# Performance work log

Hardware: AMD Instinct MI355X
Metric: run time of the kernel (lower is better)

The kernel has to match this reference:

```python
import jax, jax.numpy as jnp
import numpy as np

B, N, D = 4, 2048, 1024

def setup_inputs() -> dict:
    key = jax.random.key(0)
    ks = jax.random.split(key, 8)
    s = 1.0 / np.sqrt(D)
    return {
        "x": jax.random.normal(ks[0], (B, N, D), dtype=jnp.float32),
        "Wq": jax.random.normal(ks[1], (D, D), dtype=jnp.float32) * s,
        "bq": jnp.zeros((D,), dtype=jnp.float32),
        "Wk": jax.random.normal(ks[2], (D, D), dtype=jnp.float32) * s,
        "bk": jnp.zeros((D,), dtype=jnp.float32),
        "Wv": jax.random.normal(ks[3], (D, D), dtype=jnp.float32) * s,
        "bv": jnp.zeros((D,), dtype=jnp.float32),
        "gamma": jnp.ones((1,), dtype=jnp.float32),
    }

def reference(x, Wq, bq, Wk, bk, Wv, bv, gamma):
    d = x.shape[-1]
    delta = 1.0 / jnp.sqrt(jnp.asarray(d, dtype=x.dtype))
    # torch Linear: y = x @ W.T + b, W is [out, in]
    Q = jnp.einsum('bnd,ed->bne', x, Wq) + bq
    K = jnp.einsum('bnd,ed->bne', x, Wk) + bk
    V = jnp.einsum('bnd,ed->bne', x, Wv) + bv
    scores = jnp.einsum('bne,bme->bnm', Q, K) * delta  # [B, N, N]
    attn = jax.nn.softmax(scores, axis=-1)
    out = jnp.einsum('bnm,bme->bne', attn, V)
    return out * gamma + x
```

## Files before the change

### kernel.cpp

```cpp
#include <hip/hip_runtime.h>

typedef _Float16 f16;
typedef __attribute__((ext_vector_type(4))) _Float16 f16x4;
typedef __attribute__((ext_vector_type(8))) _Float16 f16x8;
typedef __attribute__((ext_vector_type(4))) float f32x4;

#define B_ 4
#define N_ 2048
#define D_ 1024

#define FENCE asm volatile("" ::: "memory")

__global__ __launch_bounds__(256) void k_cast_all(const float4* __restrict__ x,
                                                  const float4* __restrict__ wq,
                                                  const float4* __restrict__ wk,
                                                  const float4* __restrict__ wv,
                                                  f16x4* __restrict__ xo,
                                                  f16x4* __restrict__ wqo,
                                                  f16x4* __restrict__ wko,
                                                  f16x4* __restrict__ wvo,
                                                  float* __restrict__ rowsum) {
  int b = blockIdx.x;
  if (b >= 11264) {
    rowsum[(b - 11264) * 256 + threadIdx.x] = 0.f;
    return;
  }
  const float4* in;
  f16x4* out;
  int idx;
  if (b < 8192)       { in = x;  out = xo;  idx = b * 256 + threadIdx.x; }
  else if (b < 9216)  { in = wq; out = wqo; idx = (b - 8192) * 256 + threadIdx.x; }
  else if (b < 10240) { in = wk; out = wko; idx = (b - 9216) * 256 + threadIdx.x; }
  else                { in = wv; out = wvo; idx = (b - 10240) * 256 + threadIdx.x; }
  float4 v = in[idx];
  f16x4 o = { (_Float16)v.x, (_Float16)v.y, (_Float16)v.z, (_Float16)v.w };
  out[idx] = o;
}

__device__ __forceinline__ void stage_half(const char* g0, int ldB, int kByte,
                                           char* slot, int tid) {
#pragma unroll
  for (int r = 0; r < 2; ++r) {
    int lin = r * 8192 + tid * 16;
    int row = lin >> 7;
    int lch = ((lin >> 4) & 7) ^ (row & 7);
    const char* g = g0 + (long)row * ldB + kByte + lch * 16;
    char* l = slot + r * 8192 + ((tid >> 6) << 10);
    __builtin_amdgcn_global_load_lds(
        (const __attribute__((address_space(1))) unsigned int*)g,
        (__attribute__((address_space(3))) unsigned int*)l, 16, 0, 0);
  }
}

__device__ __forceinline__ void gemm256(const char* gA, int ldaB,
                                        const char* gB, int ldbB,
                                        int nK, char* lds, f32x4 acc[2][4][2][2]) {
  const int tid = threadIdx.x;
  const int lane = tid & 63;
  const int wave = tid >> 6;
  const int wm = wave >> 2, wn = wave & 3;
  const int quad = lane >> 4, l16 = lane & 15;
  const int l7 = l16 & 7;
  const char* gA1 = gA + (long)128 * ldaB;
  const char* gB1 = gB + (long)128 * ldbB;
  char* Abuf = lds;
  char* Bbuf = lds + 65536;
  stage_half(gA,  ldaB, 0, Abuf, tid);
  stage_half(gB,  ldbB, 0, Bbuf, tid);
  stage_half(gA1, ldaB, 0, Abuf + 16384, tid);
  stage_half(gB1, ldbB, 0, Bbuf + 16384, tid);
  for (int t = 0; t < nK; ++t) {
    const int c = t & 1;
    char* Ac = Abuf + c * 32768;
    char* Bc = Bbuf + c * 32768;
    char* An = Abuf + (c ^ 1) * 32768;
    char* Bn = Bbuf + (c ^ 1) * 32768;
    const bool st = (t + 1 < nK);
    const int kB = (t + 1) << 7;
    f16x8 bf[2][2];
#pragma unroll
    for (int ph = 0; ph < 4; ++ph) {
      const int Ah = ph & 1, Bh = ph >> 1;
      if (ph == 0)      { asm volatile("s_waitcnt vmcnt(4)" ::: "memory"); }
      else if (ph == 1) { if (st) asm volatile("s_waitcnt vmcnt(4)" ::: "memory");
                          else    asm volatile("s_waitcnt vmcnt(2)" ::: "memory"); }
      else if (ph == 2) { if (st) asm volatile("s_waitcnt vmcnt(4)" ::: "memory");
                          else    asm volatile("s_waitcnt vmcnt(0)" ::: "memory"); }
      __builtin_amdgcn_s_barrier();
      FENCE;
      f16x8 af[4][2];
      const char* Ab = Ac + Ah * 16384;
#pragma unroll
      for (int i = 0; i < 4; ++i) {
        int rA = wm * 64 + i * 16 + l16;
#pragma unroll
        for (int kk = 0; kk < 2; ++kk)
          af[i][kk] = *(const f16x8*)(Ab + rA * 128 + ((((kk << 2) | quad) ^ l7) << 4));
      }
      if (Ah == 0) {
        const char* Bb = Bc + Bh * 16384;
#pragma unroll
        for (int jn = 0; jn < 2; ++jn) {
          int rB = wn * 32 + jn * 16 + l16;
#pragma unroll
          for (int kk = 0; kk < 2; ++kk)
            bf[jn][kk] = *(const f16x8*)(Bb + rB * 128 + ((((kk << 2) | quad) ^ l7) << 4));
        }
      }
      if (st) {
        if (ph == 0)      stage_half(gA,  ldaB, kB, An, tid);
        else if (ph == 1) stage_half(gB,  ldbB, kB, Bn, tid);
        else if (ph == 2) stage_half(gA1, ldaB, kB, An + 16384, tid);
        else              stage_half(gB1, ldbB, kB, Bn + 16384, tid);
      }
      FENCE;
      __builtin_amdgcn_s_barrier();
      __builtin_amdgcn_s_setprio(1);
#pragma unroll
      for (int i = 0; i < 4; ++i)
#pragma unroll
        for (int jn = 0; jn < 2; ++jn)
#pragma unroll
          for (int kk = 0; kk < 2; ++kk)
            acc[Ah][i][Bh][jn] = __builtin_amdgcn_mfma_f32_16x16x32_f16(
                af[i][kk], bf[jn][kk], acc[Ah][i][Bh][jn], 0, 0, 0);
      __builtin_amdgcn_s_setprio(0);
    }
  }
  asm volatile("s_waitcnt vmcnt(0)" ::: "memory");
  __builtin_amdgcn_s_barrier();
  FENCE;
}

__device__ __forceinline__ void gemm_tb(const char* gA, int ldaB,
                                        const char* gB, int ldbB,
                                        int nK, char* lds, f32x4 acc[4][4]) {
  const int tid = threadIdx.x;
  const int lane = tid & 63;
  const int wave = tid >> 6;
  const int wm = wave >> 1, wn = wave & 1;
  const int quad = lane >> 4, l16 = lane & 15;
  const int l7 = l16 & 7;
  const char* gA1 = gA + (long)128 * ldaB;
  stage_half(gA,  ldaB, 0, lds, tid);
  stage_half(gA1, ldaB, 0, lds + 16384, tid);
  stage_half(gB,  ldbB, 0, lds + 32768, tid);
  stage_half(gA,  ldaB, 128, lds + 49152, tid);
  stage_half(gA1, ldaB, 128, lds + 49152 + 16384, tid);
  stage_half(gB,  ldbB, 128, lds + 49152 + 32768, tid);
  int cs = 0;
  for (int t = 0; t < nK; ++t) {
    char* Ac = lds + cs * 49152;
    char* Bc = Ac + 32768;
    int ns = cs + 2; if (ns >= 3) ns -= 3;
    char* An = lds + ns * 49152;
    const bool st = (t + 2 < nK);
    const int kB = (t + 2) << 7;
#pragma unroll
    for (int ph = 0; ph < 2; ++ph) {
      if (ph == 0) {
        if (t + 1 < nK) asm volatile("s_waitcnt vmcnt(6)" ::: "memory");
        else            asm volatile("s_waitcnt vmcnt(0)" ::: "memory");
      }
      __builtin_amdgcn_s_barrier();
      FENCE;
      f16x8 af[4], bf[4];
#pragma unroll
      for (int i = 0; i < 4; ++i) {
        int rA = wm * 64 + i * 16 + l16;
        af[i] = *(const f16x8*)(Ac + rA * 128 + ((((ph << 2) | quad) ^ l7) << 4));
      }
#pragma unroll
      for (int j = 0; j < 4; ++j) {
        int rB = wn * 64 + j * 16 + l16;
        bf[j] = *(const f16x8*)(Bc + rB * 128 + ((((ph << 2) | quad) ^ l7) << 4));
      }
      if (st) {
        if (ph == 0) { stage_half(gA,  ldaB, kB, An, tid);
                       stage_half(gA1, ldaB, kB, An + 16384, tid); }
        else         { stage_half(gB,  ldbB, kB, An + 32768, tid); }
      }
      FENCE;
      __builtin_amdgcn_s_barrier();
      __builtin_amdgcn_s_setprio(1);
#pragma unroll
      for (int i = 0; i < 4; ++i)
#pragma unroll
        for (int j = 0; j < 4; ++j)
          acc[i][j] = __builtin_amdgcn_mfma_f32_16x16x32_f16(af[i], bf[j], acc[i][j], 0, 0, 0);
      __builtin_amdgcn_s_setprio(0);
    }
    cs = cs + 1; if (cs == 3) cs = 0;
  }
  asm volatile("s_waitcnt vmcnt(0)" ::: "memory");
  __builtin_amdgcn_s_barrier();
  FENCE;
}

__global__ __launch_bounds__(512, 2) void k_qkv(const f16* __restrict__ X,
                                                const f16* __restrict__ Wq,
                                                const f16* __restrict__ Wk,
                                                const f16* __restrict__ Wv,
                                                const float* __restrict__ bq,
                                                const float* __restrict__ bk,
                                                const float* __restrict__ bv,
                                                f16* __restrict__ Q, f16* __restrict__ Ko,
                                                f16* __restrict__ Vt) {
  __shared__ __align__(16) char lds[147456];
  int fid = blockIdx.x;
  int xcd = fid & 7, k = fid >> 3;
  int rowt = xcd * 4 + (k & 3);
  int colt = k >> 2;
  int tm = rowt * 256;
  int w = colt >> 3;
  int tnl = (colt & 7) * 128;
  const f16* Wsel = (w == 0) ? Wq : (w == 1) ? Wk : Wv;
  f32x4 acc[4][4];
#pragma unroll
  for (int i = 0; i < 4; ++i)
#pragma unroll
    for (int j = 0; j < 4; ++j) acc[i][j] = (f32x4){0.f, 0.f, 0.f, 0.f};
  gemm_tb((const char*)(X + (long)tm * D_), D_ * 2,
          (const char*)(Wsel + (long)tnl * D_), D_ * 2, D_ / 64, lds, acc);
  const int tid = threadIdx.x;
  const int lane = tid & 63, wave = tid >> 6;
  const int wm = wave >> 1, wn = wave & 1;
  const int quad = lane >> 4, l16 = lane & 15;
  if (w < 2) {
    const float* bias = w ? bk : bq;
    f16* outp = w ? Ko : Q;
#pragma unroll
    for (int j = 0; j < 4; ++j) {
      int col = tnl + wn * 64 + j * 16 + l16;
      float bb = bias[col];
#pragma unroll
      for (int i = 0; i < 4; ++i) {
        int rbase = tm + wm * 64 + i * 16 + quad * 4;
#pragma unroll
        for (int r = 0; r < 4; ++r)
          outp[(long)(rbase + r) * D_ + col] = (_Float16)(acc[i][j][r] + bb);
      }
    }
  } else {
    int bidx = tm >> 11, ntok = tm & 2047;
    f16* VtB = Vt + (long)bidx * D_ * N_ + ntok;
    f16* ldsT = (f16*)lds;
#pragma unroll
    for (int j = 0; j < 4; ++j) {
      int cl = wn * 64 + j * 16 + l16;
      float bb = bv[tnl + cl];
#pragma unroll
      for (int i = 0; i < 4; ++i) {
        int rl = wm * 64 + i * 16 + quad * 4;
        f16x4 p = { (_Float16)(acc[i][j][0] + bb), (_Float16)(acc[i][j][1] + bb),
                    (_Float16)(acc[i][j][2] + bb), (_Float16)(acc[i][j][3] + bb) };
        *(f16x4*)(ldsT + cl * 264 + rl) = p;
      }
    }
    FENCE;
    __builtin_amdgcn_s_barrier();
    FENCE;
#pragma unroll
    for (int p = 0; p < 8; ++p) {
      int f = p * 16 + (tid >> 5);
      int cc = tid & 31;
      f16x8 v = *(const f16x8*)(ldsT + f * 264 + cc * 8);
      *(f16x8*)(VtB + (long)(tnl + f) * N_ + cc * 8) = v;
    }
  }
}

__global__ __launch_bounds__(512, 2) void k_scores(const f16* __restrict__ Qf,
                                                   const f16* __restrict__ Kf,
                                                   f16* __restrict__ S,
                                                   float* __restrict__ rowsum) {
  __shared__ __align__(16) char lds[131072];
  int fid = blockIdx.x;
  int xcd = fid & 7, k = fid >> 3;
  int lin = xcd * 32 + k;
  int b = lin >> 6;
  int t = lin & 63;
  int rowt = t & 7, colt = t >> 3;
  int tm = rowt * 256, tn = colt * 256;
  f32x4 acc[2][4][2][2];
#pragma unroll
  for (int Ah = 0; Ah < 2; ++Ah)
#pragma unroll
    for (int i = 0; i < 4; ++i)
#pragma unroll
      for (int Bh = 0; Bh < 2; ++Bh)
#pragma unroll
        for (int jn = 0; jn < 2; ++jn) acc[Ah][i][Bh][jn] = (f32x4){0.f, 0.f, 0.f, 0.f};
  gemm256((const char*)(Qf + (long)b * N_ * D_ + (long)tm * D_), D_ * 2,
          (const char*)(Kf + (long)b * N_ * D_ + (long)tn * D_), D_ * 2,
          D_ / 64, lds, acc);
  const int tid = threadIdx.x;
  const int lane = tid & 63, wave = tid >> 6;
  const int wm = wave >> 2, wn = wave & 3;
  const int quad = lane >> 4, l16 = lane & 15;
  f16* Sb = S + (long)b * N_ * N_;
  const float delta = 0.03125f;
  f16* ldsS = (f16*)lds;
  float rsum[2][4][4];
#pragma unroll
  for (int Ah = 0; Ah < 2; ++Ah)
#pragma unroll
    for (int i = 0; i < 4; ++i)
#pragma unroll
      for (int r = 0; r < 4; ++r) rsum[Ah][i][r] = 0.f;
#pragma unroll
  for (int Bh = 0; Bh < 2; ++Bh) {
    FENCE;
    __builtin_amdgcn_s_barrier();
    FENCE;
#pragma unroll
    for (int Ah = 0; Ah < 2; ++Ah)
#pragma unroll
      for (int i = 0; i < 4; ++i) {
        int rloc = Ah * 128 + wm * 64 + i * 16 + quad * 4;
#pragma unroll
        for (int jn = 0; jn < 2; ++jn) {
          int col = wn * 32 + jn * 16 + l16;
#pragma unroll
          for (int r = 0; r < 4; ++r) {
            float e = __expf(acc[Ah][i][Bh][jn][r] * delta);
            rsum[Ah][i][r] += e;
            ldsS[(rloc + r) * 136 + col] = (_Float16)e;
          }
        }
      }
    FENCE;
    __builtin_amdgcn_s_barrier();
    FENCE;
#pragma unroll
    for (int p = 0; p < 8; ++p) {
      int row = p * 32 + (tid >> 4);
      int cc = tid & 15;
      f16x8 v = *(const f16x8*)(ldsS + row * 136 + cc * 8);
      *(f16x8*)(Sb + (long)(tm + row) * N_ + tn + Bh * 128 + cc * 8) = v;
    }
  }
#pragma unroll
  for (int m = 1; m < 16; m <<= 1)
#pragma unroll
    for (int Ah = 0; Ah < 2; ++Ah)
#pragma unroll
      for (int i = 0; i < 4; ++i)
#pragma unroll
        for (int r = 0; r < 4; ++r) rsum[Ah][i][r] += __shfl_xor(rsum[Ah][i][r], m);
  if (l16 == 0) {
    float* rs = rowsum + (long)b * N_ + tm;
#pragma unroll
    for (int Ah = 0; Ah < 2; ++Ah)
#pragma unroll
      for (int i = 0; i < 4; ++i)
#pragma unroll
        for (int r = 0; r < 4; ++r)
          atomicAdd(rs + Ah * 128 + wm * 64 + i * 16 + quad * 4 + r, rsum[Ah][i][r]);
  }
}

__global__ __launch_bounds__(512, 2) void k_out(const f16* __restrict__ P,
                                                const f16* __restrict__ Vt,
                                                const f16* __restrict__ xf,
                                                const float* __restrict__ gamma,
                                                const float* __restrict__ rowsum,
                                                float* __restrict__ out) {
  __shared__ __align__(16) char lds[147456];
  int fid = blockIdx.x;
  int xcd = fid & 7, kq = fid >> 3;
  int lin = xcd * 32 + kq;
  int b = lin >> 6;
  int t = lin & 63;
  int rowt = t >> 3, colt = t & 7;
  int tm = rowt * 256, tn = colt * 128;
  f32x4 acc[4][4];
#pragma unroll
  for (int i = 0; i < 4; ++i)
#pragma unroll
    for (int j = 0; j < 4; ++j) acc[i][j] = (f32x4){0.f, 0.f, 0.f, 0.f};
  gemm_tb((const char*)(P + (long)b * N_ * N_ + (long)tm * N_), N_ * 2,
          (const char*)(Vt + (long)b * D_ * N_ + (long)tn * N_), N_ * 2,
          N_ / 64, lds, acc);
  const int tid = threadIdx.x;
  const int lane = tid & 63, wave = tid >> 6;
  const int wm = wave >> 1, wn = wave & 1;
  const int quad = lane >> 4, l16 = lane & 15;
  float g = gamma[0];
  float inv[4][4];
#pragma unroll
  for (int i = 0; i < 4; ++i)
#pragma unroll
    for (int r = 0; r < 4; ++r)
      inv[i][r] = g / rowsum[(long)b * N_ + tm + wm * 64 + i * 16 + quad * 4 + r];
#pragma unroll
  for (int j = 0; j < 4; ++j) {
    int col = tn + wn * 64 + j * 16 + l16;
#pragma unroll
    for (int i = 0; i < 4; ++i) {
      int rbase = tm + wm * 64 + i * 16 + quad * 4;
#pragma unroll
      for (int r = 0; r < 4; ++r) {
        long idx = (long)b * N_ * D_ + (long)(rbase + r) * D_ + col;
        out[idx] = acc[i][j][r] * inv[i][r] + (float)xf[idx];
      }
    }
  }
}

extern "C" void kernel_launch(void* const* d_in, const int* in_sizes, int n_in,
                              void* d_out, int out_size, void* d_ws, size_t ws_size,
                              hipStream_t stream) {
  const float* x  = (const float*)d_in[0];
  const float* Wq = (const float*)d_in[1];
  const float* bq = (const float*)d_in[2];
  const float* Wk = (const float*)d_in[3];
  const float* bk = (const float*)d_in[4];
  const float* Wv = (const float*)d_in[5];
  const float* bv = (const float*)d_in[6];
  const float* gamma = (const float*)d_in[7];
  float* out = (float*)d_out;
  char* ws = (char*)d_ws;

  f16* Qb  = (f16*)(ws);
  f16* Kb  = (f16*)(ws + (16u << 20));
  f16* Vt  = (f16*)(ws + (32u << 20));
  f16* Xb  = (f16*)(ws + (48u << 20));
  f16* Wqb = (f16*)(ws + (64u << 20));
  f16* Wkb = (f16*)(ws + (66u << 20));
  f16* Wvb = (f16*)(ws + (68u << 20));
  f16* S   = (f16*)(ws + (64u << 20));
  float* rowsum = (float*)(ws + (96u << 20));

  k_cast_all<<<11296, 256, 0, stream>>>((const float4*)x, (const float4*)Wq,
                                        (const float4*)Wk, (const float4*)Wv,
                                        (f16x4*)Xb, (f16x4*)Wqb, (f16x4*)Wkb, (f16x4*)Wvb,
                                        rowsum);
  k_qkv<<<768, 512, 0, stream>>>(Xb, Wqb, Wkb, Wvb, bq, bk, bv, Qb, Kb, Vt);
  k_scores<<<256, 512, 0, stream>>>(Qb, Kb, S, rowsum);
  k_out<<<256, 512, 0, stream>>>(S, Vt, Xb, gamma, rowsum, out);
}
```

Baseline: 250.1 us.

## Use 256x256 tiles for QKV and split-K output GEMM with atomics

Drops the 256x128 triple-buffered gemm_tb and moves k_qkv and k_out onto the 256x256 gemm256 path, halving the QKV grid. k_out now splits K into two halves (ks) so it keeps 256 blocks, and accumulates into the output with atomicAdd; the residual is added only by the ks==0 half. The output buffer is zeroed in the cast kernel through extra blocks. gemm256 now caches both A halves in registers, so the A fragments are not reloaded from LDS in phases 2-3. The cost is more fp32 atomic traffic on the output, an extra pass to zero it, and higher register pressure.

```diff
diff --git a/kernel.cpp b/kernel.cpp
--- a/kernel.cpp
+++ b/kernel.cpp
@@ -19,8 +19,13 @@
                                                   f16x4* __restrict__ wqo,
                                                   f16x4* __restrict__ wko,
                                                   f16x4* __restrict__ wvo,
-                                                  float* __restrict__ rowsum) {
+                                                  float* __restrict__ rowsum,
+                                                  float4* __restrict__ outz) {
   int b = blockIdx.x;
+  if (b >= 11296) {
+    outz[(b - 11296) * 256 + threadIdx.x] = (float4){0.f, 0.f, 0.f, 0.f};
+    return;
+  }
   if (b >= 11264) {
     rowsum[(b - 11264) * 256 + threadIdx.x] = 0.f;
     return;
@@ -77,6 +82,7 @@
     char* Bn = Bbuf + (c ^ 1) * 32768;
     const bool st = (t + 1 < nK);
     const int kB = (t + 1) << 7;
+    f16x8 afc[2][4][2];
     f16x8 bf[2][2];
 #pragma unroll
     for (int ph = 0; ph < 4; ++ph) {
@@ -88,14 +94,15 @@
                           else    asm volatile("s_waitcnt vmcnt(0)" ::: "memory"); }
       __builtin_amdgcn_s_barrier();
       FENCE;
-      f16x8 af[4][2];
-      const char* Ab = Ac + Ah * 16384;
-#pragma unroll
-      for (int i = 0; i < 4; ++i) {
-        int rA = wm * 64 + i * 16 + l16;
-#pragma unroll
-        for (int kk = 0; kk < 2; ++kk)
-          af[i][kk] = *(const f16x8*)(Ab + rA * 128 + ((((kk << 2) | quad) ^ l7) << 4));
+      if (ph < 2) {
+        const char* Ab = Ac + ph * 16384;
+#pragma unroll
+        for (int i = 0; i < 4; ++i) {
+          int rA = wm * 64 + i * 16 + l16;
+#pragma unroll
+          for (int kk = 0; kk < 2; ++kk)
+            afc[ph][i][kk] = *(const f16x8*)(Ab + rA * 128 + ((((kk << 2) | quad) ^ l7) << 4));
+        }
       }
       if (Ah == 0) {
         const char* Bb = Bc + Bh * 16384;
@@ -123,74 +130,9 @@
 #pragma unroll
           for (int kk = 0; kk < 2; ++kk)
             acc[Ah][i][Bh][jn] = __builtin_amdgcn_mfma_f32_16x16x32_f16(
-                af[i][kk], bf[jn][kk], acc[Ah][i][Bh][jn], 0, 0, 0);
+                afc[Ah][i][kk], bf[jn][kk], acc[Ah][i][Bh][jn], 0, 0, 0);
       __builtin_amdgcn_s_setprio(0);
     }
-  }
-  asm volatile("s_waitcnt vmcnt(0)" ::: "memory");
-  __builtin_amdgcn_s_barrier();
-  FENCE;
-}
-
-__device__ __forceinline__ void gemm_tb(const char* gA, int ldaB,
-                                        const char* gB, int ldbB,
-                                        int nK, char* lds, f32x4 acc[4][4]) {
-  const int tid = threadIdx.x;
-  const int lane = tid & 63;
-  const int wave = tid >> 6;
-  const int wm = wave >> 1, wn = wave & 1;
-  const int quad = lane >> 4, l16 = lane & 15;
-  const int l7 = l16 & 7;
-  const char* gA1 = gA + (long)128 * ldaB;
-  stage_half(gA,  ldaB, 0, lds, tid);
-  stage_half(gA1, ldaB, 0, lds + 16384, tid);
-  stage_half(gB,  ldbB, 0, lds + 32768, tid);
-  stage_half(gA,  ldaB, 128, lds + 49152, tid);
-  stage_half(gA1, ldaB, 128, lds + 49152 + 16384, tid);
-  stage_half(gB,  ldbB, 128, lds + 49152 + 32768, tid);
-  int cs = 0;
-  for (int t = 0; t < nK; ++t) {
-    char* Ac = lds + cs * 49152;
-    char* Bc = Ac + 32768;
-    int ns = cs + 2; if (ns >= 3) ns -= 3;
-    char* An = lds + ns * 49152;
-    const bool st = (t + 2 < nK);
-    const int kB = (t + 2) << 7;
-#pragma unroll
-    for (int ph = 0; ph < 2; ++ph) {
-      if (ph == 0) {
-        if (t + 1 < nK) asm volatile("s_waitcnt vmcnt(6)" ::: "memory");
-        else            asm volatile("s_waitcnt vmcnt(0)" ::: "memory");
-      }
-      __builtin_amdgcn_s_barrier();
-      FENCE;
-      f16x8 af[4], bf[4];
-#pragma unroll
-      for (int i = 0; i < 4; ++i) {
-        int rA = wm * 64 + i * 16 + l16;
-        af[i] = *(const f16x8*)(Ac + rA * 128 + ((((ph << 2) | quad) ^ l7) << 4));
-      }
-#pragma unroll
-      for (int j = 0; j < 4; ++j) {
-        int rB = wn * 64 + j * 16 + l16;
-        bf[j] = *(const f16x8*)(Bc + rB * 128 + ((((ph << 2) | quad) ^ l7) << 4));
-      }
-      if (st) {
-        if (ph == 0) { stage_half(gA,  ldaB, kB, An, tid);
-                       stage_half(gA1, ldaB, kB, An + 16384, tid); }
-        else         { stage_half(gB,  ldbB, kB, An + 32768, tid); }
-      }
-      FENCE;
-      __builtin_amdgcn_s_barrier();
-      __builtin_amdgcn_s_setprio(1);
-#pragma unroll
-      for (int i = 0; i < 4; ++i)
-#pragma unroll
-        for (int j = 0; j < 4; ++j)
-          acc[i][j] = __builtin_amdgcn_mfma_f32_16x16x32_f16(af[i], bf[j], acc[i][j], 0, 0, 0);
-      __builtin_amdgcn_s_setprio(0);
-    }
-    cs = cs + 1; if (cs == 3) cs = 0;
   }
   asm volatile("s_waitcnt vmcnt(0)" ::: "memory");
   __builtin_amdgcn_s_barrier();
@@ -206,66 +148,84 @@
                                                 const float* __restrict__ bv,
                                                 f16* __restrict__ Q, f16* __restrict__ Ko,
                                                 f16* __restrict__ Vt) {
-  __shared__ __align__(16) char lds[147456];
+  __shared__ __align__(16) char lds[131072];
   int fid = blockIdx.x;
   int xcd = fid & 7, k = fid >> 3;
   int rowt = xcd * 4 + (k & 3);
   int colt = k >> 2;
   int tm = rowt * 256;
-  int w = colt >> 3;
-  int tnl = (colt & 7) * 128;
+  int w = colt >> 2;
+  int tn = (colt & 3) * 256;
   const f16* Wsel = (w == 0) ? Wq : (w == 1) ? Wk : Wv;
-  f32x4 acc[4][4];
-#pragma unroll
-  for (int i = 0; i < 4; ++i)
-#pragma unroll
-    for (int j = 0; j < 4; ++j) acc[i][j] = (f32x4){0.f, 0.f, 0.f, 0.f};
-  gemm_tb((const char*)(X + (long)tm * D_), D_ * 2,
-          (const char*)(Wsel + (long)tnl * D_), D_ * 2, D_ / 64, lds, acc);
+  f32x4 acc[2][4][2][2];
+#pragma unroll
+  for (int Ah = 0; Ah < 2; ++Ah)
+#pragma unroll
+    for (int i = 0; i < 4; ++i)
+#pragma unroll
+      for (int Bh = 0; Bh < 2; ++Bh)
+#pragma unroll
+        for (int jn = 0; jn < 2; ++jn) acc[Ah][i][Bh][jn] = (f32x4){0.f, 0.f, 0.f, 0.f};
+  gemm256((const char*)(X + (long)tm * D_), D_ * 2,
+          (const char*)(Wsel + (long)tn * D_), D_ * 2, D_ / 64, lds, acc);
   const int tid = threadIdx.x;
   const int lane = tid & 63, wave = tid >> 6;
-  const int wm = wave >> 1, wn = wave & 1;
+  const int wm = wave >> 2, wn = wave & 3;
   const int quad = lane >> 4, l16 = lane & 15;
   if (w < 2) {
     const float* bias = w ? bk : bq;
     f16* outp = w ? Ko : Q;
 #pragma unroll
-    for (int j = 0; j < 4; ++j) {
-      int col = tnl + wn * 64 + j * 16 + l16;
-      float bb = bias[col];
-#pragma unroll
-      for (int i = 0; i < 4; ++i) {
-        int rbase = tm + wm * 64 + i * 16 + quad * 4;
-#pragma unroll
-        for (int r = 0; r < 4; ++r)
-          outp[(long)(rbase + r) * D_ + col] = (_Float16)(acc[i][j][r] + bb);
-      }
-    }
+    for (int Bh = 0; Bh < 2; ++Bh)
+#pragma unroll
+      for (int jn = 0; jn < 2; ++jn) {
+        int col = tn + Bh * 128 + wn * 32 + jn * 16 + l16;
+        float bb = bias[col];
+#pragma unroll
+        for (int Ah = 0; Ah < 2; ++Ah)
+#pragma unroll
+          for (int i = 0; i < 4; ++i) {
+            int rbase = tm + Ah * 128 + wm * 64 + i * 16 + quad * 4;
+#pragma unroll
+            for (int r = 0; r < 4; ++r)
+              outp[(long)(rbase + r) * D_ + col] = (_Float16)(acc[Ah][i][Bh][jn][r] + bb);
+          }
+      }
   } else {
     int bidx = tm >> 11, ntok = tm & 2047;
     f16* VtB = Vt + (long)bidx * D_ * N_ + ntok;
     f16* ldsT = (f16*)lds;
 #pragma unroll
-    for (int j = 0; j < 4; ++j) {
-      int cl = wn * 64 + j * 16 + l16;
-      float bb = bv[tnl + cl];
-#pragma unroll
-      for (int i = 0; i < 4; ++i) {
-        int rl = wm * 64 + i * 16 + quad * 4;
-        f16x4 p = { (_Float16)(acc[i][j][0] + bb), (_Float16)(acc[i][j][1] + bb),
-                    (_Float16)(acc[i][j][2] + bb), (_Float16)(acc[i][j][3] + bb) };
-        *(f16x4*)(ldsT + cl * 264 + rl) = p;
-      }
-    }
-    FENCE;
-    __builtin_amdgcn_s_barrier();
-    FENCE;
-#pragma unroll
-    for (int p = 0; p < 8; ++p) {
-      int f = p * 16 + (tid >> 5);
-      int cc = tid & 31;
-      f16x8 v = *(const f16x8*)(ldsT + f * 264 + cc * 8);
-      *(f16x8*)(VtB + (long)(tnl + f) * N_ + cc * 8) = v;
+    for (int pass = 0; pass < 2; ++pass) {
+      FENCE;
+      __builtin_amdgcn_s_barrier();
+      FENCE;
+#pragma unroll
+      for (int jn = 0; jn < 2; ++jn) {
+        int fl = wn * 32 + jn * 16 + l16;
+        float bb = bv[tn + pass * 128 + fl];
+#pragma unroll
+        for (int Ah = 0; Ah < 2; ++Ah)
+#pragma unroll
+          for (int i = 0; i < 4; ++i) {
+            int rl = Ah * 128 + wm * 64 + i * 16 + quad * 4;
+            f16x4 p = { (_Float16)(acc[Ah][i][pass][jn][0] + bb),
+                        (_Float16)(acc[Ah][i][pass][jn][1] + bb),
+                        (_Float16)(acc[Ah][i][pass][jn][2] + bb),
+                        (_Float16)(acc[Ah][i][pass][jn][3] + bb) };
+            *(f16x4*)(ldsT + fl * 264 + rl) = p;
+          }
+      }
+      FENCE;
+      __builtin_amdgcn_s_barrier();
+      FENCE;
+#pragma unroll
+      for (int p = 0; p < 8; ++p) {
+        int f = p * 16 + (tid >> 5);
+        int cc = tid & 31;
+        f16x8 v = *(const f16x8*)(ldsT + f * 264 + cc * 8);
+        *(f16x8*)(VtB + (long)(tn + pass * 128 + f) * N_ + cc * 8) = v;
+      }
     }
   }
 }
@@ -366,46 +326,60 @@
                                                 const float* __restrict__ gamma,
                                                 const float* __restrict__ rowsum,
                                                 float* __restrict__ out) {
-  __shared__ __align__(16) char lds[147456];
+  __shared__ __align__(16) char lds[131072];
   int fid = blockIdx.x;
   int xcd = fid & 7, kq = fid >> 3;
   int lin = xcd * 32 + kq;
-  int b = lin >> 6;
-  int t = lin & 63;
-  int rowt = t >> 3, colt = t & 7;
-  int tm = rowt * 256, tn = colt * 128;
-  f32x4 acc[4][4];
-#pragma unroll
-  for (int i = 0; i < 4; ++i)
-#pragma unroll
-    for (int j = 0; j < 4; ++j) acc[i][j] = (f32x4){0.f, 0.f, 0.f, 0.f};
-  gemm_tb((const char*)(P + (long)b * N_ * N_ + (long)tm * N_), N_ * 2,
-          (const char*)(Vt + (long)b * D_ * N_ + (long)tn * N_), N_ * 2,
-          N_ / 64, lds, acc);
+  int ks = lin >> 7;
+  int rem = lin & 127;
+  int b = rem >> 5;
+  int t = rem & 31;
+  int rowt = t >> 2, colt = t & 3;
+  int tm = rowt * 256, tn = colt * 256;
+  f32x4 acc[2][4][2][2];
+#pragma unroll
+  for (int Ah = 0; Ah < 2; ++Ah)
+#pragma unroll
+    for (int i = 0; i < 4; ++i)
+#pragma unroll
+      for (int Bh = 0; Bh < 2; ++Bh)
+#pragma unroll
+        for (int jn = 0; jn < 2; ++jn) acc[Ah][i][Bh][jn] = (f32x4){0.f, 0.f, 0.f, 0.f};
+  gemm256((const char*)(P + (long)b * N_ * N_ + (long)tm * N_ + ks * 1024), N_ * 2,
+          (const char*)(Vt + (long)b * D_ * N_ + (long)tn * N_ + ks * 1024), N_ * 2,
+          1024 / 64, lds, acc);
   const int tid = threadIdx.x;
   const int lane = tid & 63, wave = tid >> 6;
-  const int wm = wave >> 1, wn = wave & 1;
+  const int wm = wave >> 2, wn = wave & 3;
   const int quad = lane >> 4, l16 = lane & 15;
   float g = gamma[0];
-  float inv[4][4];
-#pragma unroll
-  for (int i = 0; i < 4; ++i)
-#pragma unroll
-    for (int r = 0; r < 4; ++r)
-      inv[i][r] = g / rowsum[(long)b * N_ + tm + wm * 64 + i * 16 + quad * 4 + r];
-#pragma unroll
-  for (int j = 0; j < 4; ++j) {
-    int col = tn + wn * 64 + j * 16 + l16;
-#pragma unroll
-    for (int i = 0; i < 4; ++i) {
-      int rbase = tm + wm * 64 + i * 16 + quad * 4;
-#pragma unroll
-      for (int r = 0; r < 4; ++r) {
-        long idx = (long)b * N_ * D_ + (long)(rbase + r) * D_ + col;
-        out[idx] = acc[i][j][r] * inv[i][r] + (float)xf[idx];
-      }
+  float inv[2][4][4];
+#pragma unroll
+  for (int Ah = 0; Ah < 2; ++Ah)
+#pragma unroll
+    for (int i = 0; i < 4; ++i)
+#pragma unroll
+      for (int r = 0; r < 4; ++r)
+        inv[Ah][i][r] = g / rowsum[(long)b * N_ + tm + Ah * 128 + wm * 64 + i * 16 + quad * 4 + r];
+#pragma unroll
+  for (int Bh = 0; Bh < 2; ++Bh)
+#pragma unroll
+    for (int jn = 0; jn < 2; ++jn) {
+      int col = tn + Bh * 128 + wn * 32 + jn * 16 + l16;
+#pragma unroll
+      for (int Ah = 0; Ah < 2; ++Ah)
+#pragma unroll
+        for (int i = 0; i < 4; ++i) {
+          int rbase = tm + Ah * 128 + wm * 64 + i * 16 + quad * 4;
+#pragma unroll
+          for (int r = 0; r < 4; ++r) {
+            long idx = (long)b * N_ * D_ + (long)(rbase + r) * D_ + col;
+            float v = acc[Ah][i][Bh][jn][r] * inv[Ah][i][r];
+            if (ks == 0) v += (float)xf[idx];
+            atomicAdd(out + idx, v);
+          }
+        }
     }
-  }
 }
 
 extern "C" void kernel_launch(void* const* d_in, const int* in_sizes, int n_in,
@@ -432,11 +406,11 @@
   f16* S   = (f16*)(ws + (64u << 20));
   float* rowsum = (float*)(ws + (96u << 20));
 
-  k_cast_all<<<11296, 256, 0, stream>>>((const float4*)x, (const float4*)Wq,
+  k_cast_all<<<19488, 256, 0, stream>>>((const float4*)x, (const float4*)Wq,
                                         (const float4*)Wk, (const float4*)Wv,
                                         (f16x4*)Xb, (f16x4*)Wqb, (f16x4*)Wkb, (f16x4*)Wvb,
-                                        rowsum);
-  k_qkv<<<768, 512, 0, stream>>>(Xb, Wqb, Wkb, Wvb, bq, bk, bv, Qb, Kb, Vt);
+                                        rowsum, (float4*)out);
+  k_qkv<<<384, 512, 0, stream>>>(Xb, Wqb, Wkb, Wvb, bq, bk, bv, Qb, Kb, Vt);
   k_scores<<<256, 512, 0, stream>>>(Qb, Kb, S, rowsum);
   k_out<<<256, 512, 0, stream>>>(S, Vt, Xb, gamma, rowsum, out);
 }
```

New measurement: 299.3 us. 19.7% more time.
